# Optimization experiments

Hardware: AMD Instinct MI355X
Metric: run time of the kernel (lower is better)

## Reference

```python
import jax, jax.numpy as jnp
import numpy as np

B, T, C = 4, 2048, 1024
H, D = 16, 64


def setup_inputs() -> dict:
    key = jax.random.key(0)
    ks = jax.random.split(key, 6)
    s = 0.02
    return {
        "x": jax.random.normal(ks[0], (B, T, C), dtype=jnp.float32),
        "wq": jax.random.normal(ks[1], (H, C, D), dtype=jnp.float32) * s,
        "wk": jax.random.normal(ks[2], (H, C, D), dtype=jnp.float32) * s,
        "wv": jax.random.normal(ks[3], (H, C, D), dtype=jnp.float32) * s,
        "w_proj": jax.random.normal(ks[4], (C, C), dtype=jnp.float32) * s,
        "b_proj": jnp.zeros((C,), dtype=jnp.float32),
    }


def reference(x, wq, wk, wv, w_proj, b_proj):
    b, t, c = x.shape
    # per-head projections, vectorized over heads: [B,T,C] x [H,C,D] -> [B,H,T,D]
    q = jnp.einsum("btc,hcd->bhtd", x, wq)
    k = jnp.einsum("btc,hcd->bhtd", x, wk)
    v = jnp.einsum("btc,hcd->bhtd", x, wv)
    # NOTE: original scales by C**-0.5 where C = n_embd (not head_size)
    scale = jnp.asarray(c, x.dtype) ** -0.5
    scores = jnp.einsum("bhtd,bhsd->bhts", q, k) * scale  # [B,H,T,T]
    causal = jnp.tril(jnp.ones((t, t), dtype=bool))
    scores = jnp.where(causal, scores, jnp.finfo(x.dtype).min)
    wei = jax.nn.softmax(scores, axis=-1)
    out = jnp.einsum("bhts,bhsd->bhtd", wei, v)  # [B,H,T,D]
    out = out.transpose(0, 2, 1, 3).reshape(b, t, c)  # concat heads
    return out @ w_proj + b_proj
```

## Files before the change

kernel.cpp:

```cpp
#include <hip/hip_runtime.h>
#include <hip/hip_bf16.h>
#include <stdint.h>

#define B_ 4
#define T_ 2048
#define C_ 1024
#define H_ 16
#define D_ 64

typedef __attribute__((ext_vector_type(8))) short bf16x8;
typedef __attribute__((ext_vector_type(4))) short short4v;
typedef __attribute__((ext_vector_type(4))) float f32x4;

static __device__ __forceinline__ short f2bf(float f) {
    union { float f; unsigned u; } v; v.f = f;
    unsigned r = v.u + 0x7fffu + ((v.u >> 16) & 1u);
    return (short)(r >> 16);
}

static __device__ __forceinline__ float fast_exp2(float x) {
    float r;
    asm("v_exp_f32 %0, %1" : "=v"(r) : "v"(x));
    return r;
}

#define GLD_LDS16(g, l) __builtin_amdgcn_global_load_lds( \
    (const __attribute__((address_space(1))) void*)(g),   \
    (__attribute__((address_space(3))) void*)(l), 16, 0, 0)

#define QSCALE 0.04508422f

__global__ void pack_x(const float* __restrict__ x, short* __restrict__ xb) {
    int t = blockIdx.x * blockDim.x + threadIdx.x;
    const float* src = x + (size_t)t * 8;
    float4 v0 = *(const float4*)src;
    float4 v1 = *(const float4*)(src + 4);
    bf16x8 o;
    o[0] = f2bf(v0.x); o[1] = f2bf(v0.y); o[2] = f2bf(v0.z); o[3] = f2bf(v0.w);
    o[4] = f2bf(v1.x); o[5] = f2bf(v1.y); o[6] = f2bf(v1.z); o[7] = f2bf(v1.w);
    *(bf16x8*)(xb + (size_t)t * 8) = o;
}

__global__ void pack_wqkv2(const float* __restrict__ wq, const float* __restrict__ wk,
                           const float* __restrict__ wv, short* __restrict__ out) {
    __shared__ short tile[64][72];
    const int qh = blockIdx.y;
    const int qkv = qh >> 4, h = qh & 15;
    const int c0 = blockIdx.x * 64;
    const float* w = ((qkv == 0) ? wq : (qkv == 1) ? wk : wv) + (size_t)h * (C_ * D_);
    const int t = threadIdx.x;
    const int r = t >> 2;
    const int dc = (t & 3) * 16;

    const float* src = w + (size_t)(c0 + r) * D_ + dc;
#pragma unroll
    for (int j = 0; j < 4; ++j) {
        float4 v = *(const float4*)(src + j * 4);
        short4v s;
        s[0] = f2bf(v.x); s[1] = f2bf(v.y); s[2] = f2bf(v.z); s[3] = f2bf(v.w);
        *(short4v*)&tile[r][dc + j * 4] = s;
    }
    __syncthreads();

    const int d = t >> 2;
    const int cc = (t & 3) * 16;
    bf16x8 o0, o1;
#pragma unroll
    for (int j = 0; j < 8; ++j) {
        o0[j] = tile[cc + j][d];
        o1[j] = tile[cc + 8 + j][d];
    }
    short* dst = out + ((size_t)qkv * 1024 + h * 64 + d) * C_ + c0 + cc;
    *(bf16x8*)dst = o0;
    *(bf16x8*)(dst + 8) = o1;
}

__global__ void pack_wproj2(const float* __restrict__ wp, short* __restrict__ out) {
    __shared__ short tile[64][72];
    const int c0 = blockIdx.x * 64;
    const int n0 = blockIdx.y * 64;
    const int t = threadIdx.x;
    const int r = t >> 2;
    const int nc = (t & 3) * 16;

    const float* src = wp + (size_t)(c0 + r) * C_ + n0 + nc;
#pragma unroll
    for (int j = 0; j < 4; ++j) {
        float4 v = *(const float4*)(src + j * 4);
        short4v s;
        s[0] = f2bf(v.x); s[1] = f2bf(v.y); s[2] = f2bf(v.z); s[3] = f2bf(v.w);
        *(short4v*)&tile[r][nc + j * 4] = s;
    }
    __syncthreads();

    const int n = t >> 2;
    const int cc = (t & 3) * 16;
    bf16x8 o0, o1;
#pragma unroll
    for (int j = 0; j < 8; ++j) {
        o0[j] = tile[cc + j][n];
        o1[j] = tile[cc + 8 + j][n];
    }
    short* dst = out + (size_t)(n0 + n) * C_ + c0 + cc;
    *(bf16x8*)dst = o0;
    *(bf16x8*)(dst + 8) = o1;
}

template<int MODE>
__global__ __launch_bounds__(256)
void gemm_lds(const short* __restrict__ A, const short* __restrict__ Bt,
              void* __restrict__ Cptr, short* __restrict__ vtptr,
              const float* __restrict__ bias, int M, int N, int K) {
    __shared__ short As[128 * 64];
    __shared__ short Bs[128 * 64];
    const int tid = threadIdx.x;
    const int lane = tid & 63, wid = tid >> 6;
    const int wr = wid >> 1, wc = wid & 1;
    const int l15 = lane & 15, l4 = lane >> 4;
    const int m0 = blockIdx.y * 128, n0 = blockIdx.x * 128;

    f32x4 acc[4][4] = {};

    for (int k0 = 0; k0 < K; k0 += 64) {
#pragma unroll
        for (int p = 0; p < 4; ++p) {
            int e = p * 256 + tid;
            int r = e >> 3, pc = e & 7;
            int lc = pc ^ (r & 7);
            GLD_LDS16(A  + (size_t)(m0 + r) * K + k0 + lc * 8, As + e * 8);
            GLD_LDS16(Bt + (size_t)(n0 + r) * K + k0 + lc * 8, Bs + e * 8);
        }
        __syncthreads();

#pragma unroll
        for (int kk = 0; kk < 2; ++kk) {
            bf16x8 af[4], bfr[4];
#pragma unroll
            for (int m = 0; m < 4; ++m) {
                int row = wr * 64 + m * 16 + l15;
                int pc = (kk * 4 + l4) ^ (row & 7);
                af[m] = *(const bf16x8*)(As + row * 64 + pc * 8);
            }
#pragma unroll
            for (int n = 0; n < 4; ++n) {
                int row = wc * 64 + n * 16 + l15;
                int pc = (kk * 4 + l4) ^ (row & 7);
                bfr[n] = *(const bf16x8*)(Bs + row * 64 + pc * 8);
            }
#pragma unroll
            for (int m = 0; m < 4; ++m)
#pragma unroll
                for (int n = 0; n < 4; ++n)
                    acc[m][n] = __builtin_amdgcn_mfma_f32_16x16x32_bf16(af[m], bfr[n], acc[m][n], 0, 0, 0);
        }
        __syncthreads();
    }

#pragma unroll
    for (int m = 0; m < 4; ++m) {
        int row_base = m0 + wr * 64 + m * 16 + l4 * 4;
#pragma unroll
        for (int n = 0; n < 4; ++n) {
            int col = n0 + wc * 64 + n * 16 + l15;
            if (MODE == 1) {
#pragma unroll
                for (int r = 0; r < 4; ++r)
                    ((float*)Cptr)[(size_t)(row_base + r) * N + col] =
                        acc[m][n][r] + bias[col];
            } else {
                if (col < 2048) {
                    float q = (col < 1024) ? QSCALE : 1.0f;
#pragma unroll
                    for (int r = 0; r < 4; ++r)
                        ((short*)Cptr)[(size_t)(row_base + r) * 2048 + col] =
                            f2bf(acc[m][n][r] * q);
                } else {
                    int cm = col - 2048;
                    int bq = row_base >> 11, t = row_base & 2047;
                    short4v s;
                    s[0] = f2bf(acc[m][n][0]); s[1] = f2bf(acc[m][n][1]);
                    s[2] = f2bf(acc[m][n][2]); s[3] = f2bf(acc[m][n][3]);
                    *(short4v*)(vtptr + ((size_t)bq * 1024 + cm) * 2048 + t) = s;
                }
            }
        }
    }
}

__device__ __forceinline__ void softmax_phase(
    f32x4 S[4], f32x4 O[4], float* mrow, float* srow,
    int qrow0, int s0, bool diag, int l15, int l4, short* ps) {
    float pmax[4];
#pragma unroll
    for (int r = 0; r < 4; ++r) pmax[r] = -1e30f;
#pragma unroll
    for (int n = 0; n < 4; ++n) {
#pragma unroll
        for (int r = 0; r < 4; ++r) {
            float v = S[n][r];
            if (diag) {
                int scol = s0 + n * 16 + l15;
                if (scol > qrow0 + r) v = -1e30f;
            }
            S[n][r] = v;
            pmax[r] = fmaxf(pmax[r], v);
        }
    }
#pragma unroll
    for (int r = 0; r < 4; ++r) {
        float v = pmax[r];
        v = fmaxf(v, __shfl_xor(v, 1));
        v = fmaxf(v, __shfl_xor(v, 2));
        v = fmaxf(v, __shfl_xor(v, 4));
        v = fmaxf(v, __shfl_xor(v, 8));
        pmax[r] = v;
    }
    int ok = (pmax[0] <= mrow[0] + 8.0f) & (pmax[1] <= mrow[1] + 8.0f) &
             (pmax[2] <= mrow[2] + 8.0f) & (pmax[3] <= mrow[3] + 8.0f);
    if (!__all(ok)) {
#pragma unroll
        for (int r = 0; r < 4; ++r) {
            float mnew = fmaxf(mrow[r], pmax[r]);
            float fr = fast_exp2(mrow[r] - mnew);
            mrow[r] = mnew;
            srow[r] *= fr;
#pragma unroll
            for (int n = 0; n < 4; ++n) O[n][r] *= fr;
        }
    }
    float psum[4];
#pragma unroll
    for (int r = 0; r < 4; ++r) psum[r] = 0.0f;
#pragma unroll
    for (int n = 0; n < 4; ++n) {
#pragma unroll
        for (int r = 0; r < 4; ++r) {
            float p = fast_exp2(S[n][r] - mrow[r]);
            psum[r] += p;
            ps[(l4 * 4 + r) * 72 + n * 16 + l15] = f2bf(p);
        }
    }
#pragma unroll
    for (int r = 0; r < 4; ++r) {
        float v = psum[r];
        v += __shfl_xor(v, 1);
        v += __shfl_xor(v, 2);
        v += __shfl_xor(v, 4);
        v += __shfl_xor(v, 8);
        srow[r] += v;
    }
}

__global__ __launch_bounds__(256)
void attn_v16(const short* __restrict__ qk, const short* __restrict__ vt,
              short* __restrict__ out) {
    const int pi = blockIdx.x;
    const int bh = blockIdx.y;
    const int b = bh >> 4;
    const int h = bh & 15;
    const int qA0 = pi * 64;
    const int qB0 = (31 - pi) * 64;
    const int ntA = pi + 1;
    const int ntB = 32 - pi;
    const int tid = threadIdx.x;
    const int wave = tid >> 6;
    const int lane = tid & 63;
    const int l15 = lane & 15, l4 = lane >> 4;

    __shared__ short Vt[2][64][64];
    __shared__ short Ps[4][2][16][72];

    const size_t rs = 2 * C_;
    const short* qbA = qk + ((size_t)b * T_ + qA0) * rs + h * 64;
    const short* qbB = qk + ((size_t)b * T_ + qB0) * rs + h * 64;
    const short* kb  = qk + (size_t)b * T_ * rs + 1024 + h * 64;
    const short* vtb = vt + (size_t)bh * 64 * T_;

    bf16x8 aqA0 = *(const bf16x8*)(qbA + (size_t)(wave * 16 + l15) * rs + l4 * 8);
    bf16x8 aqA1 = *(const bf16x8*)(qbA + (size_t)(wave * 16 + l15) * rs + 32 + l4 * 8);
    bf16x8 aqB0 = *(const bf16x8*)(qbB + (size_t)(wave * 16 + l15) * rs + l4 * 8);
    bf16x8 aqB1 = *(const bf16x8*)(qbB + (size_t)(wave * 16 + l15) * rs + 32 + l4 * 8);

    f32x4 OA[4] = {}, OB[4] = {};
    float mA[4], sA[4], mB[4], sB[4];
#pragma unroll
    for (int r = 0; r < 4; ++r) { mA[r] = mB[r] = -1e30f; sA[r] = sB[r] = 0.0f; }

    short* psB = &Ps[wave][0][0][0];
    short* psA = &Ps[wave][1][0][0];
    const int qrB = qB0 + wave * 16 + l4 * 4;
    const int qrA = qA0 + wave * 16 + l4 * 4;

    const int sr = tid >> 3;
    const int spc = tid & 7;

    auto stage = [&](int slot, int s0) {
#pragma unroll
        for (int p = 0; p < 2; ++p) {
            int e = p * 256 + tid;
            int r = (p == 0) ? sr : (sr + 32);
            int lc = spc ^ (r & 7);
            GLD_LDS16(vtb + (size_t)r * T_ + s0 + lc * 8,
                      &Vt[slot][0][0] + e * 8);
        }
    };

    auto qk_sm = [&](int s0, bool actA) {
        bf16x8 bk0[4], bk1[4];
#pragma unroll
        for (int n = 0; n < 4; ++n) {
            const short* kr = kb + (size_t)(s0 + n * 16 + l15) * rs;
            bk0[n] = *(const bf16x8*)(kr + l4 * 8);
            bk1[n] = *(const bf16x8*)(kr + 32 + l4 * 8);
        }
        f32x4 S[4];
#pragma unroll
        for (int n = 0; n < 4; ++n) {
            f32x4 z = {};
            z = __builtin_amdgcn_mfma_f32_16x16x32_bf16(aqB0, bk0[n], z, 0, 0, 0);
            S[n] = __builtin_amdgcn_mfma_f32_16x16x32_bf16(aqB1, bk1[n], z, 0, 0, 0);
        }
        softmax_phase(S, OB, mB, sB, qrB, s0, s0 == qB0, l15, l4, psB);
        if (actA) {
            f32x4 SA[4];
#pragma unroll
            for (int n = 0; n < 4; ++n) {
                f32x4 z = {};
                z = __builtin_amdgcn_mfma_f32_16x16x32_bf16(aqA0, bk0[n], z, 0, 0, 0);
                SA[n] = __builtin_amdgcn_mfma_f32_16x16x32_bf16(aqA1, bk1[n], z, 0, 0, 0);
            }
            softmax_phase(SA, OA, mA, sA, qrA, s0, s0 == qA0, l15, l4, psA);
        }
    };

    auto pv = [&](int slot, bool actA) {
        bf16x8 apB0 = *(const bf16x8*)(psB + l15 * 72 + l4 * 8);
        bf16x8 apB1 = *(const bf16x8*)(psB + l15 * 72 + 32 + l4 * 8);
        const int x7 = l15 & 7;
#pragma unroll
        for (int n = 0; n < 4; ++n) {
            const short* vrow = &Vt[slot][n * 16 + l15][0];
            bf16x8 bv0 = *(const bf16x8*)(vrow + ((l4 ^ x7) * 8));
            bf16x8 bv1 = *(const bf16x8*)(vrow + (((l4 + 4) ^ x7) * 8));
            OB[n] = __builtin_amdgcn_mfma_f32_16x16x32_bf16(apB0, bv0, OB[n], 0, 0, 0);
            OB[n] = __builtin_amdgcn_mfma_f32_16x16x32_bf16(apB1, bv1, OB[n], 0, 0, 0);
        }
        if (actA) {
            bf16x8 apA0 = *(const bf16x8*)(psA + l15 * 72 + l4 * 8);
            bf16x8 apA1 = *(const bf16x8*)(psA + l15 * 72 + 32 + l4 * 8);
#pragma unroll
            for (int n = 0; n < 4; ++n) {
                const short* vrow = &Vt[slot][n * 16 + l15][0];
                bf16x8 bv0 = *(const bf16x8*)(vrow + ((l4 ^ x7) * 8));
                bf16x8 bv1 = *(const bf16x8*)(vrow + (((l4 + 4) ^ x7) * 8));
                OA[n] = __builtin_amdgcn_mfma_f32_16x16x32_bf16(apA0, bv0, OA[n], 0, 0, 0);
                OA[n] = __builtin_amdgcn_mfma_f32_16x16x32_bf16(apA1, bv1, OA[n], 0, 0, 0);
            }
        }
    };

    const int npair = ntB & ~1;
    for (int t = 0; t < npair; t += 2) {
        const int s0 = t * 64;
        __syncthreads();

        stage(0, s0);
        stage(1, s0 + 64);

        qk_sm(s0, t < ntA);

        __syncthreads();

        pv(0, t < ntA);
        qk_sm(s0 + 64, t + 1 < ntA);

        asm volatile("s_waitcnt lgkmcnt(0)" ::: "memory");
        __builtin_amdgcn_sched_barrier(0);

        pv(1, t + 1 < ntA);
    }

    if (ntB & 1) {
        const int s0 = npair * 64;
        __syncthreads();
        stage(0, s0);
        qk_sm(s0, npair < ntA);
        __syncthreads();
        pv(0, npair < ntA);
    }

#pragma unroll
    for (int r = 0; r < 4; ++r) {
        int rowB = qB0 + wave * 16 + l4 * 4 + r;
        int rowA = qA0 + wave * 16 + l4 * 4 + r;
        float invB = 1.0f / sB[r];
        float invA = 1.0f / sA[r];
        size_t obB = ((size_t)b * T_ + rowB) * C_ + h * 64;
        size_t obA = ((size_t)b * T_ + rowA) * C_ + h * 64;
#pragma unroll
        for (int n = 0; n < 4; ++n) {
            out[obB + n * 16 + l15] = f2bf(OB[n][r] * invB);
            out[obA + n * 16 + l15] = f2bf(OA[n][r] * invA);
        }
    }
}

extern "C" void kernel_launch(void* const* d_in, const int* in_sizes, int n_in,
                              void* d_out, int out_size, void* d_ws, size_t ws_size,
                              hipStream_t stream) {
    const float* x     = (const float*)d_in[0];
    const float* wq    = (const float*)d_in[1];
    const float* wk    = (const float*)d_in[2];
    const float* wv    = (const float*)d_in[3];
    const float* wproj = (const float*)d_in[4];
    const float* bproj = (const float*)d_in[5];
    float* out = (float*)d_out;

    short* wqkv_t  = (short*)d_ws;
    short* wproj_t = wqkv_t + 3072 * 1024;
    short* qk_b    = wproj_t + 1024 * 1024;
    short* vt_b    = qk_b + (size_t)8192 * 2048;
    short* attn_b  = vt_b + (size_t)64 * 64 * 2048;
    short* xb      = attn_b;

    pack_x<<<4096, 256, 0, stream>>>(x, xb);
    pack_wqkv2<<<dim3(16, 48), 256, 0, stream>>>(wq, wk, wv, wqkv_t);
    pack_wproj2<<<dim3(16, 16), 256, 0, stream>>>(wproj, wproj_t);

    gemm_lds<2><<<dim3(24, 64), 256, 0, stream>>>(
        xb, wqkv_t, qk_b, vt_b, nullptr, 8192, 3072, 1024);

    attn_v16<<<dim3(16, 64), 256, 0, stream>>>(qk_b, vt_b, attn_b);

    gemm_lds<1><<<dim3(8, 64), 256, 0, stream>>>(
        attn_b, wproj_t, out, nullptr, bproj, 8192, 1024, 1024);
}
```

Before: 271.3 us.

## Widen attention blocks to 8 waves covering 128-row query tile pairs

```diff
diff --git a/kernel.cpp b/kernel.cpp
--- a/kernel.cpp
+++ b/kernel.cpp
@@ -251,24 +251,26 @@
     }
 }
 
-__global__ __launch_bounds__(256)
-void attn_v16(const short* __restrict__ qk, const short* __restrict__ vt,
+__global__ __launch_bounds__(512)
+void attn_v17(const short* __restrict__ qk, const short* __restrict__ vt,
               short* __restrict__ out) {
     const int pi = blockIdx.x;
     const int bh = blockIdx.y;
     const int b = bh >> 4;
     const int h = bh & 15;
-    const int qA0 = pi * 64;
-    const int qB0 = (31 - pi) * 64;
-    const int ntA = pi + 1;
-    const int ntB = 32 - pi;
     const int tid = threadIdx.x;
     const int wave = tid >> 6;
     const int lane = tid & 63;
     const int l15 = lane & 15, l4 = lane >> 4;
 
+    const int qA0 = pi * 128 + wave * 16;
+    const int qB0 = (15 - pi) * 128 + wave * 16;
+    const int lastA = 2 * pi + (wave >> 2);
+    const int lastB = 30 - 2 * pi + (wave >> 2);
+    const int nt = 32 - 2 * pi;
+
     __shared__ short Vt[2][64][64];
-    __shared__ short Ps[4][2][16][72];
+    __shared__ short Ps[8][2][16][72];
 
     const size_t rs = 2 * C_;
     const short* qbA = qk + ((size_t)b * T_ + qA0) * rs + h * 64;
@@ -276,10 +278,10 @@
     const short* kb  = qk + (size_t)b * T_ * rs + 1024 + h * 64;
     const short* vtb = vt + (size_t)bh * 64 * T_;
 
-    bf16x8 aqA0 = *(const bf16x8*)(qbA + (size_t)(wave * 16 + l15) * rs + l4 * 8);
-    bf16x8 aqA1 = *(const bf16x8*)(qbA + (size_t)(wave * 16 + l15) * rs + 32 + l4 * 8);
-    bf16x8 aqB0 = *(const bf16x8*)(qbB + (size_t)(wave * 16 + l15) * rs + l4 * 8);
-    bf16x8 aqB1 = *(const bf16x8*)(qbB + (size_t)(wave * 16 + l15) * rs + 32 + l4 * 8);
+    bf16x8 aqA0 = *(const bf16x8*)(qbA + (size_t)l15 * rs + l4 * 8);
+    bf16x8 aqA1 = *(const bf16x8*)(qbA + (size_t)l15 * rs + 32 + l4 * 8);
+    bf16x8 aqB0 = *(const bf16x8*)(qbB + (size_t)l15 * rs + l4 * 8);
+    bf16x8 aqB1 = *(const bf16x8*)(qbB + (size_t)l15 * rs + 32 + l4 * 8);
 
     f32x4 OA[4] = {}, OB[4] = {};
     float mA[4], sA[4], mB[4], sB[4];
@@ -288,24 +290,19 @@
 
     short* psB = &Ps[wave][0][0][0];
     short* psA = &Ps[wave][1][0][0];
-    const int qrB = qB0 + wave * 16 + l4 * 4;
-    const int qrA = qA0 + wave * 16 + l4 * 4;
+    const int qrB = qB0 + l4 * 4;
+    const int qrA = qA0 + l4 * 4;
 
     const int sr = tid >> 3;
     const int spc = tid & 7;
 
     auto stage = [&](int slot, int s0) {
-#pragma unroll
-        for (int p = 0; p < 2; ++p) {
-            int e = p * 256 + tid;
-            int r = (p == 0) ? sr : (sr + 32);
-            int lc = spc ^ (r & 7);
-            GLD_LDS16(vtb + (size_t)r * T_ + s0 + lc * 8,
-                      &Vt[slot][0][0] + e * 8);
-        }
+        int lc = spc ^ (sr & 7);
+        GLD_LDS16(vtb + (size_t)sr * T_ + s0 + lc * 8,
+                  &Vt[slot][0][0] + tid * 8);
     };
 
-    auto qk_sm = [&](int s0, bool actA) {
+    auto qk_sm = [&](int s0, bool actB, bool diagB, bool actA, bool diagA) {
         bf16x8 bk0[4], bk1[4];
 #pragma unroll
         for (int n = 0; n < 4; ++n) {
@@ -313,14 +310,16 @@
             bk0[n] = *(const bf16x8*)(kr + l4 * 8);
             bk1[n] = *(const bf16x8*)(kr + 32 + l4 * 8);
         }
-        f32x4 S[4];
-#pragma unroll
-        for (int n = 0; n < 4; ++n) {
-            f32x4 z = {};
-            z = __builtin_amdgcn_mfma_f32_16x16x32_bf16(aqB0, bk0[n], z, 0, 0, 0);
-            S[n] = __builtin_amdgcn_mfma_f32_16x16x32_bf16(aqB1, bk1[n], z, 0, 0, 0);
-        }
-        softmax_phase(S, OB, mB, sB, qrB, s0, s0 == qB0, l15, l4, psB);
+        if (actB) {
+            f32x4 S[4];
+#pragma unroll
+            for (int n = 0; n < 4; ++n) {
+                f32x4 z = {};
+                z = __builtin_amdgcn_mfma_f32_16x16x32_bf16(aqB0, bk0[n], z, 0, 0, 0);
+                S[n] = __builtin_amdgcn_mfma_f32_16x16x32_bf16(aqB1, bk1[n], z, 0, 0, 0);
+            }
+            softmax_phase(S, OB, mB, sB, qrB, s0, diagB, l15, l4, psB);
+        }
         if (actA) {
             f32x4 SA[4];
 #pragma unroll
@@ -329,21 +328,23 @@
                 z = __builtin_amdgcn_mfma_f32_16x16x32_bf16(aqA0, bk0[n], z, 0, 0, 0);
                 SA[n] = __builtin_amdgcn_mfma_f32_16x16x32_bf16(aqA1, bk1[n], z, 0, 0, 0);
             }
-            softmax_phase(SA, OA, mA, sA, qrA, s0, s0 == qA0, l15, l4, psA);
+            softmax_phase(SA, OA, mA, sA, qrA, s0, diagA, l15, l4, psA);
         }
     };
 
-    auto pv = [&](int slot, bool actA) {
-        bf16x8 apB0 = *(const bf16x8*)(psB + l15 * 72 + l4 * 8);
-        bf16x8 apB1 = *(const bf16x8*)(psB + l15 * 72 + 32 + l4 * 8);
+    auto pv = [&](int slot, bool actB, bool actA) {
         const int x7 = l15 & 7;
-#pragma unroll
-        for (int n = 0; n < 4; ++n) {
-            const short* vrow = &Vt[slot][n * 16 + l15][0];
-            bf16x8 bv0 = *(const bf16x8*)(vrow + ((l4 ^ x7) * 8));
-            bf16x8 bv1 = *(const bf16x8*)(vrow + (((l4 + 4) ^ x7) * 8));
-            OB[n] = __builtin_amdgcn_mfma_f32_16x16x32_bf16(apB0, bv0, OB[n], 0, 0, 0);
-            OB[n] = __builtin_amdgcn_mfma_f32_16x16x32_bf16(apB1, bv1, OB[n], 0, 0, 0);
+        if (actB) {
+            bf16x8 apB0 = *(const bf16x8*)(psB + l15 * 72 + l4 * 8);
+            bf16x8 apB1 = *(const bf16x8*)(psB + l15 * 72 + 32 + l4 * 8);
+#pragma unroll
+            for (int n = 0; n < 4; ++n) {
+                const short* vrow = &Vt[slot][n * 16 + l15][0];
+                bf16x8 bv0 = *(const bf16x8*)(vrow + ((l4 ^ x7) * 8));
+                bf16x8 bv1 = *(const bf16x8*)(vrow + (((l4 + 4) ^ x7) * 8));
+                OB[n] = __builtin_amdgcn_mfma_f32_16x16x32_bf16(apB0, bv0, OB[n], 0, 0, 0);
+                OB[n] = __builtin_amdgcn_mfma_f32_16x16x32_bf16(apB1, bv1, OB[n], 0, 0, 0);
+            }
         }
         if (actA) {
             bf16x8 apA0 = *(const bf16x8*)(psA + l15 * 72 + l4 * 8);
@@ -359,40 +360,30 @@
         }
     };
 
-    const int npair = ntB & ~1;
-    for (int t = 0; t < npair; t += 2) {
+    for (int t = 0; t < nt; t += 2) {
         const int s0 = t * 64;
         __syncthreads();
 
         stage(0, s0);
         stage(1, s0 + 64);
 
-        qk_sm(s0, t < ntA);
+        qk_sm(s0, t <= lastB, t == lastB, t <= lastA, t == lastA);
 
         __syncthreads();
 
-        pv(0, t < ntA);
-        qk_sm(s0 + 64, t + 1 < ntA);
+        pv(0, t <= lastB, t <= lastA);
+        qk_sm(s0 + 64, t + 1 <= lastB, t + 1 == lastB, t + 1 <= lastA, t + 1 == lastA);
 
         asm volatile("s_waitcnt lgkmcnt(0)" ::: "memory");
         __builtin_amdgcn_sched_barrier(0);
 
-        pv(1, t + 1 < ntA);
-    }
-
-    if (ntB & 1) {
-        const int s0 = npair * 64;
-        __syncthreads();
-        stage(0, s0);
-        qk_sm(s0, npair < ntA);
-        __syncthreads();
-        pv(0, npair < ntA);
+        pv(1, t + 1 <= lastB, t + 1 <= lastA);
     }
 
 #pragma unroll
     for (int r = 0; r < 4; ++r) {
-        int rowB = qB0 + wave * 16 + l4 * 4 + r;
-        int rowA = qA0 + wave * 16 + l4 * 4 + r;
+        int rowB = qB0 + l4 * 4 + r;
+        int rowA = qA0 + l4 * 4 + r;
         float invB = 1.0f / sB[r];
         float invA = 1.0f / sA[r];
         size_t obB = ((size_t)b * T_ + rowB) * C_ + h * 64;
@@ -430,7 +421,7 @@
     gemm_lds<2><<<dim3(24, 64), 256, 0, stream>>>(
         xb, wqkv_t, qk_b, vt_b, nullptr, 8192, 3072, 1024);
 
-    attn_v16<<<dim3(16, 64), 256, 0, stream>>>(qk_b, vt_b, attn_b);
+    attn_v17<<<dim3(8, 64), 512, 0, stream>>>(qk_b, vt_b, attn_b);
 
     gemm_lds<1><<<dim3(8, 64), 256, 0, stream>>>(
         attn_b, wproj_t, out, nullptr, bproj, 8192, 1024, 1024);
```

Measured after the change: 338.9 us. 24.9% more time.
